# Kernel tuning notes

Hardware: AMD Instinct MI355X
Metric: run time of the kernel (lower is better)

Reference implementation:

```python
import jax, jax.numpy as jnp
import numpy as np

N_NODES = 100000; N_EDGES = 800000
N_SVC = 51200; E_SVC = 409600
B = 1024; OUT = 50; HID = 128; EMB = 64; VOCAB = 100
BN_EPS = 1e-5


def _bn(x, g, b):
    # BatchNorm1d in training mode: biased batch statistics
    m = x.mean(0)
    v = x.var(0)
    return (x - m) * jax.lax.rsqrt(v + BN_EPS) * g + b


def _gin(x, ei, W1, b1, bng, bnb, W2, b2, eps, n):
    # GINConv: nn((1+eps)*x + sum_{j->i} x_j), aggregate source feats at target ei[1]
    agg = jax.ops.segment_sum(x[ei[0]], ei[1], num_segments=n)
    h = (1.0 + eps) * x + agg
    h = _bn(h @ W1 + b1, bng, bnb)
    return jax.nn.relu(h) @ W2 + b2


def _gcn(x, ei, ew, W, b, n):
    # GCNConv with edge weights: add self loops (w=1), symmetric normalization
    xw = x @ W
    loop = jnp.arange(n)
    row = jnp.concatenate([ei[0], loop])
    col = jnp.concatenate([ei[1], loop])
    w = jnp.concatenate([ew, jnp.ones((n,), ew.dtype)])
    deg = jax.ops.segment_sum(w, col, num_segments=n)
    dinv = jnp.where(deg > 0, jax.lax.rsqrt(deg), 0.0)
    norm = dinv[row] * w * dinv[col]
    return jax.ops.segment_sum(norm[:, None] * xw[row], col, num_segments=n) + b


def setup_inputs() -> dict:
    key = jax.random.key(0)
    ks = jax.random.split(key, 48)
    p = lambda k, s: jax.random.normal(k, s, jnp.float32) * 0.05
    H2 = 2 * HID
    inp = dict(
        node_ids=jax.random.randint(ks[0], (N_NODES,), 0, VOCAB),
        node_feats=jax.random.normal(ks[1], (N_NODES, 6), jnp.float32),
        edge_index=jax.random.randint(ks[2], (2, N_EDGES), 0, N_NODES),
        svc_ids=jax.random.randint(ks[3], (N_SVC,), 0, VOCAB),
        svc_feats=jax.random.normal(ks[4], (N_SVC, 4), jnp.float32),
        edge_index_service=jax.random.randint(ks[5], (2, E_SVC), 0, N_SVC),
        edge_attr_service=jax.random.uniform(ks[6], (E_SVC,), jnp.float32),
        batch=jnp.sort(jax.random.randint(ks[7], (N_NODES,), 0, B)),
        num_graphs=B,
        out_channels=OUT,
        emb_node=p(ks[8], (VOCAB, EMB)),
        emb_svc=p(ks[9], (VOCAB, EMB)),
        # GIN layer 0 (in = EMB + 6)
        g0_W1=p(ks[10], (EMB + 6, H2)), g0_b1=jnp.zeros((H2,), jnp.float32),
        g0_bng1=jnp.ones((H2,), jnp.float32), g0_bnb1=jnp.zeros((H2,), jnp.float32),
        g0_W2=p(ks[11], (H2, HID)), g0_b2=jnp.zeros((HID,), jnp.float32),
        g0_eps=jnp.zeros((), jnp.float32),
        bn0_g=jnp.ones((HID,), jnp.float32), bn0_b=jnp.zeros((HID,), jnp.float32),
        # GIN layer 1 (in = HID)
        g1_W1=p(ks[12], (HID, H2)), g1_b1=jnp.zeros((H2,), jnp.float32),
        g1_bng1=jnp.ones((H2,), jnp.float32), g1_bnb1=jnp.zeros((H2,), jnp.float32),
        g1_W2=p(ks[13], (H2, HID)), g1_b2=jnp.zeros((HID,), jnp.float32),
        g1_eps=jnp.zeros((), jnp.float32),
        bn1_g=jnp.ones((HID,), jnp.float32), bn1_b=jnp.zeros((HID,), jnp.float32),
        node_lin_W=p(ks[14], (HID, HID)), node_lin_b=jnp.zeros((HID,), jnp.float32),
        # GCN layer 0 (in = EMB + 4)
        c0_W=p(ks[15], (EMB + 4, H2)), c0_b=jnp.zeros((H2,), jnp.float32),
        cbn0_g=jnp.ones((H2,), jnp.float32), cbn0_b=jnp.zeros((H2,), jnp.float32),
        # GCN layer 1 (in = 2*HID)
        c1_W=p(ks[16], (H2, H2)), c1_b=jnp.zeros((H2,), jnp.float32),
        cbn1_g=jnp.ones((H2,), jnp.float32), cbn1_b=jnp.zeros((H2,), jnp.float32),
        svc_lin_W=p(ks[17], (H2, HID)), svc_lin_b=jnp.zeros((HID,), jnp.float32),
    )
    return inp


def reference(node_feats, svc_feats, edge_attr_service, emb_node, emb_svc,
              g0_W1, g0_b1, g0_bng1, g0_bnb1, g0_W2, g0_b2, g0_eps, bn0_g, bn0_b,
              g1_W1, g1_b1, g1_bng1, g1_bnb1, g1_W2, g1_b2, g1_eps, bn1_g, bn1_b,
              node_lin_W, node_lin_b,
              c0_W, c0_b, cbn0_g, cbn0_b, c1_W, c1_b, cbn1_g, cbn1_b,
              svc_lin_W, svc_lin_b,
              node_ids, svc_ids, edge_index, edge_index_service, batch,
              num_graphs, out_channels):
    n = node_feats.shape[0]
    ns = svc_feats.shape[0]
    # node branch: embedding(col 0) ++ 6 float cols, 2 GIN layers
    x = jnp.concatenate([emb_node[node_ids], node_feats], axis=-1)
    x = jax.nn.relu(_bn(_gin(x, edge_index, g0_W1, g0_b1, g0_bng1, g0_bnb1,
                             g0_W2, g0_b2, g0_eps, n), bn0_g, bn0_b))
    x = jax.nn.relu(_bn(_gin(x, edge_index, g1_W1, g1_b1, g1_bng1, g1_bnb1,
                             g1_W2, g1_b2, g1_eps, n), bn1_g, bn1_b))
    # service branch: embedding ++ 4 qos cols, 2 GCN layers (isServices=True)
    xs = jnp.concatenate([emb_svc[svc_ids], svc_feats], axis=-1)
    xs = jax.nn.relu(_bn(_gcn(xs, edge_index_service, edge_attr_service, c0_W, c0_b, ns),
                         cbn0_g, cbn0_b))
    xs = jax.nn.relu(_bn(_gcn(xs, edge_index_service, edge_attr_service, c1_W, c1_b, ns),
                         cbn1_g, cbn1_b))
    xs = xs @ svc_lin_W + svc_lin_b
    x = x @ node_lin_W + node_lin_b
    # scatter-mean pooling over graphs
    cnt = jax.ops.segment_sum(jnp.ones((n,), x.dtype), batch, num_segments=num_graphs)
    xg = jax.ops.segment_sum(x, batch, num_segments=num_graphs) / jnp.clip(cnt, 1.0)[:, None]
    # scatter-mean over service slots: indices [0..out-1] repeated per graph
    svc_batch = jnp.tile(jnp.arange(out_channels), ns // out_channels)
    scnt = jax.ops.segment_sum(jnp.ones((ns,), xs.dtype), svc_batch, num_segments=out_channels)
    xsg = jax.ops.segment_sum(xs, svc_batch, num_segments=out_channels) / jnp.clip(scnt, 1.0)[:, None]
    return jax.nn.sigmoid(xg @ xsg.T)
```

## Files before the change

### kernel.cpp

```cpp
#include <hip/hip_runtime.h>
#include <hip/hip_bf16.h>
#include <cstddef>
#include <cstdint>

typedef __hip_bfloat16 bf16;
typedef __attribute__((ext_vector_type(8))) short short8;
typedef __attribute__((ext_vector_type(4))) float floatx4;

static __device__ __forceinline__ float b2f(bf16 v) { return __bfloat162float(v); }

static __device__ __forceinline__ short f2bf(float f) {
    unsigned u = __float_as_uint(f);
    unsigned r = u + 0x7FFF + ((u >> 16) & 1);
    return (short)(r >> 16);
}
static __device__ __forceinline__ float bf2f(short h) {
    return __uint_as_float(((unsigned)(unsigned short)h) << 16);
}
static __device__ __forceinline__ float loadf(const void* p, int mode, size_t i) {
    if (mode == 1) return b2f(((const bf16*)p)[i]);
    if (mode == 2) return ((const float*)p)[i];
    return 0.f;
}

#define NCONV 35
struct DetArgs { const void* src[NCONV]; int n[NCONV]; };

__global__ void detect_all(DetArgs a, int* __restrict__ modes) {
    int b = blockIdx.x;
    int n = a.n[b];
    const unsigned short* w = (const unsigned short*)a.src[b];
    __shared__ int cz, cbad, cevz, codz;
    if (threadIdx.x == 0) { cz = 0; cbad = 0; cevz = 0; codz = 0; }
    __syncthreads();
    int K = n < 2048 ? n : 2048;
    int z = 0, bad = 0, evz = 0, odz = 0;
    for (int i = threadIdx.x; i < K; i += blockDim.x) {
        unsigned short v = w[i];
        int e = (v >> 7) & 0xFF;
        bool isz = (v & 0x7FFF) == 0;
        if (isz) { z++; if (i & 1) odz++; else evz++; }
        else if (e < 91 || e > 140) bad++;
    }
    atomicAdd(&cz, z); atomicAdd(&cbad, bad);
    atomicAdd(&cevz, evz); atomicAdd(&codz, odz);
    __syncthreads();
    if (threadIdx.x == 0) {
        int mode;
        if (cz >= K) mode = 0;
        else if (cbad * 16 > K) mode = 2;
        else if (cevz * 4 > K && codz * 16 < K) mode = 2;
        else mode = 1;
        modes[b] = mode;
    }
}

struct WtArgs {
    const void* W[8]; short* wt[8];
    int midx[8]; int KW[8]; int ldw[8]; int Kpad[8]; int N[8];
};
__global__ void wt_build_all(WtArgs a, const int* __restrict__ modes) {
    int e = blockIdx.y;
    int n = blockIdx.x; if (n >= a.N[e]) return;
    int k = threadIdx.x; if (k >= a.Kpad[e]) return;
    float v = (k < a.KW[e]) ? loadf(a.W[e], modes[a.midx[e]], (size_t)k * a.ldw[e] + n) : 0.f;
    a.wt[e][(size_t)n * a.Kpad[e] + k] = f2bf(v);
}

__global__ void build_feat_bf16(const void* __restrict__ emb, const int* __restrict__ ids,
                                const void* __restrict__ feats, const int* __restrict__ modes,
                                int eidx, int fidx, unsigned short* __restrict__ P,
                                int nf, int Ws) {
    int i = blockIdx.x;
    int d = threadIdx.x;
    if (d >= Ws) return;
    float v;
    if (d < 64)           v = loadf(emb, modes[eidx], (size_t)ids[i] * 64 + d);
    else if (d < 64 + nf) v = loadf(feats, modes[fidx], (size_t)i * nf + (d - 64));
    else                  v = 0.f;
    P[(size_t)i * Ws + d] = (unsigned short)f2bf(v);
}

__global__ void csr_count(const int* __restrict__ dst, int nE, int* __restrict__ cnt) {
    int e = blockIdx.x * blockDim.x + threadIdx.x;
    if (e < nE) atomicAdd(&cnt[dst[e]], 1);
}

__global__ __launch_bounds__(256) void scan_part(const int* __restrict__ cnt, int n,
                                                 int* __restrict__ bsum) {
    __shared__ int red[256];
    int blk = blockIdx.x, t = threadIdx.x;
    int base = blk * 1024 + t * 4;
    int s = 0;
    #pragma unroll
    for (int k = 0; k < 4; ++k) { int i = base + k; if (i < n) s += cnt[i]; }
    red[t] = s;
    __syncthreads();
    for (int off = 128; off > 0; off >>= 1) {
        if (t < off) red[t] += red[t + off];
        __syncthreads();
    }
    if (t == 0) bsum[blk] = red[0];
}

__global__ __launch_bounds__(128) void scan_mid(int* __restrict__ bsum, int nb,
                                                int* __restrict__ rowptr, int n) {
    __shared__ int sh[128];
    int t = threadIdx.x;
    int v = (t < nb) ? bsum[t] : 0;
    sh[t] = v;
    __syncthreads();
    for (int off = 1; off < 128; off <<= 1) {
        int u = (t >= off) ? sh[t - off] : 0;
        __syncthreads();
        sh[t] += u;
        __syncthreads();
    }
    if (t < nb) bsum[t] = sh[t] - v;
    if (t == 127) rowptr[n] = sh[127];
}

__global__ __launch_bounds__(256) void scan_fin(const int* __restrict__ cnt, int n,
                                                const int* __restrict__ bsum,
                                                int* __restrict__ rowptr, int* __restrict__ cursor) {
    __shared__ int sh[256];
    int blk = blockIdx.x, t = threadIdx.x;
    int base = blk * 1024 + t * 4;
    int v[4], s = 0;
    #pragma unroll
    for (int k = 0; k < 4; ++k) { int i = base + k; v[k] = (i < n) ? cnt[i] : 0; s += v[k]; }
    sh[t] = s;
    __syncthreads();
    for (int off = 1; off < 256; off <<= 1) {
        int u = (t >= off) ? sh[t - off] : 0;
        __syncthreads();
        sh[t] += u;
        __syncthreads();
    }
    int run = sh[t] - s + bsum[blk];
    #pragma unroll
    for (int k = 0; k < 4; ++k) {
        int i = base + k;
        if (i < n) { rowptr[i] = run; cursor[i] = run; run += v[k]; }
    }
}

__global__ void csr_fill(const int* __restrict__ src, const int* __restrict__ dst,
                         const void* __restrict__ w, const int* __restrict__ modes, int widx,
                         const float* __restrict__ dinv, int nE, int* __restrict__ cursor,
                         int* __restrict__ adj, short* __restrict__ adjw) {
    int e = blockIdx.x * blockDim.x + threadIdx.x;
    if (e < nE) {
        int s = src[e];
        int pos = atomicAdd(&cursor[dst[e]], 1);
        adj[pos] = s;
        if (adjw) adjw[pos] = f2bf(dinv[s] * loadf(w, modes[widx], e));
    }
}

__global__ __launch_bounds__(256) void gin_gather_bf16(
        const unsigned short* __restrict__ P, const int* __restrict__ rowptr,
        const int* __restrict__ adj, const void* __restrict__ eps,
        const int* __restrict__ modes, int eidx,
        const float* __restrict__ bnsc, const float* __restrict__ bnsh,
        unsigned short* __restrict__ Po, int Ws, int nN) {
    int W8 = Ws >> 3;
    int g = threadIdx.x >> 4;
    int l = threadIdx.x & 15;
    int i = blockIdx.x * 16 + g;
    if (i >= nN || l >= W8) return;
    float epsv = 1.0f + loadf(eps, modes[eidx], 0);
    float sc[8], sh[8];
    bool bn = bnsc != nullptr;
    if (bn) {
        *(float4*)&sc[0] = *(const float4*)(bnsc + l * 8);
        *(float4*)&sc[4] = *(const float4*)(bnsc + l * 8 + 4);
        *(float4*)&sh[0] = *(const float4*)(bnsh + l * 8);
        *(float4*)&sh[4] = *(const float4*)(bnsh + l * 8 + 4);
    }
    int lo = rowptr[i], hi = rowptr[i + 1];
    float acc[8] = {};
    for (int p = lo; p < hi; ++p) {
        short8 v = *(const short8*)(P + (size_t)adj[p] * Ws + l * 8);
        #pragma unroll
        for (int j = 0; j < 8; ++j) {
            float y = bf2f(v[j]);
            if (bn) y = fmaxf(fmaf(y, sc[j], sh[j]), 0.f);
            acc[j] += y;
        }
    }
    size_t o = (size_t)i * Ws + l * 8;
    short8 sv = *(const short8*)(P + o);
    short8 r;
    #pragma unroll
    for (int j = 0; j < 8; ++j) {
        float y = bf2f(sv[j]);
        if (bn) y = fmaxf(fmaf(y, sc[j], sh[j]), 0.f);
        r[j] = f2bf(acc[j] + epsv * y);
    }
    *(short8*)(Po + o) = r;
}

__global__ __launch_bounds__(256) void gcn_gather(
        const float* __restrict__ xw, const int* __restrict__ rowptr,
        const int* __restrict__ adj, const short* __restrict__ adjw,
        const float* __restrict__ dinv, const void* __restrict__ bias,
        const int* __restrict__ modes, int bidx, float* __restrict__ out, int nS) {
    int g = threadIdx.x >> 6;
    int l = threadIdx.x & 63;
    int i = blockIdx.x * 4 + g;
    if (i >= nS) return;
    float di = dinv[i];
    int bmode = modes[bidx];
    size_t o = (size_t)i * 256 + (l << 2);
    float4 self = *(const float4*)(xw + o);
    float4 acc;
    float dd = di * di;
    acc.x = self.x * dd + loadf(bias, bmode, (l << 2) + 0);
    acc.y = self.y * dd + loadf(bias, bmode, (l << 2) + 1);
    acc.z = self.z * dd + loadf(bias, bmode, (l << 2) + 2);
    acc.w = self.w * dd + loadf(bias, bmode, (l << 2) + 3);
    int lo = rowptr[i], hi = rowptr[i + 1];
    int p = lo;
    for (; p + 1 < hi; p += 2) {
        int s0 = adj[p], s1 = adj[p + 1];
        float w0 = di * bf2f(adjw[p]), w1 = di * bf2f(adjw[p + 1]);
        float4 v0 = *(const float4*)(xw + (size_t)s0 * 256 + (l << 2));
        float4 v1 = *(const float4*)(xw + (size_t)s1 * 256 + (l << 2));
        acc.x += w0 * v0.x + w1 * v1.x;
        acc.y += w0 * v0.y + w1 * v1.y;
        acc.z += w0 * v0.z + w1 * v1.z;
        acc.w += w0 * v0.w + w1 * v1.w;
    }
    if (p < hi) {
        float w0 = di * bf2f(adjw[p]);
        float4 v0 = *(const float4*)(xw + (size_t)adj[p] * 256 + (l << 2));
        acc.x += w0 * v0.x; acc.y += w0 * v0.y;
        acc.z += w0 * v0.z; acc.w += w0 * v0.w;
    }
    *(float4*)(out + o) = acc;
}

__global__ __launch_bounds__(256) void gemm_mfma(
        const void* __restrict__ A, int afmt, int ldk,
        const float* __restrict__ bnsc, const float* __restrict__ bnsh,
        const short* __restrict__ Wt,
        const void* __restrict__ bias, const int* __restrict__ modes, int bias_midx,
        float* __restrict__ outF, unsigned short* __restrict__ oB,
        float* __restrict__ stats, int M, int N, int ksteps, int bf_out) {
    int tid  = threadIdx.x;
    int wv   = tid >> 6, lane = tid & 63;
    int m16  = lane & 15, q = lane >> 4;
    int bm   = blockIdx.y * 128 + wv * 32;
    int n0   = blockIdx.x * 128;
    int r0 = min(bm + m16, M - 1);
    int r1 = min(bm + 16 + m16, M - 1);
    const short8* ba0 = (const short8*)((const short*)A + (size_t)r0 * ldk + q * 8);
    const short8* ba1 = (const short8*)((const short*)A + (size_t)r1 * ldk + q * 8);
    const float*  fa0 = (const float*)A + (size_t)r0 * ldk + q * 8;
    const float*  fa1 = (const float*)A + (size_t)r1 * ldk + q * 8;
    const short8* pb[8];
    #pragma unroll
    for (int nt = 0; nt < 8; ++nt)
        pb[nt] = (const short8*)(Wt + (size_t)(n0 + nt * 16 + m16) * ldk + q * 8);

    floatx4 acc[2][8];
    #pragma unroll
    for (int mt = 0; mt < 2; ++mt)
        #pragma unroll
        for (int nt = 0; nt < 8; ++nt)
            acc[mt][nt] = (floatx4){0.f, 0.f, 0.f, 0.f};

    bool bn = bnsc != nullptr;
    for (int ks = 0; ks < ksteps; ++ks) {
        int idx = ks * 4;
        short8 a0, a1;
        if (afmt == 0 && !bn) {
            a0 = ba0[idx];
            a1 = ba1[idx];
        } else {
            float v0[8], v1[8];
            if (afmt == 0) {
                short8 u0 = ba0[idx], u1 = ba1[idx];
                #pragma unroll
                for (int j = 0; j < 8; ++j) { v0[j] = bf2f(u0[j]); v1[j] = bf2f(u1[j]); }
            } else {
                *(float4*)&v0[0] = *(const float4*)(fa0 + ks * 32);
                *(float4*)&v0[4] = *(const float4*)(fa0 + ks * 32 + 4);
                *(float4*)&v1[0] = *(const float4*)(fa1 + ks * 32);
                *(float4*)&v1[4] = *(const float4*)(fa1 + ks * 32 + 4);
            }
            if (bn) {
                int c0 = ks * 32 + q * 8;
                float scv[8], shv[8];
                *(float4*)&scv[0] = *(const float4*)(bnsc + c0);
                *(float4*)&scv[4] = *(const float4*)(bnsc + c0 + 4);
                *(float4*)&shv[0] = *(const float4*)(bnsh + c0);
                *(float4*)&shv[4] = *(const float4*)(bnsh + c0 + 4);
                #pragma unroll
                for (int j = 0; j < 8; ++j) {
                    v0[j] = fmaxf(fmaf(v0[j], scv[j], shv[j]), 0.f);
                    v1[j] = fmaxf(fmaf(v1[j], scv[j], shv[j]), 0.f);
                }
            }
            #pragma unroll
            for (int j = 0; j < 8; ++j) { a0[j] = f2bf(v0[j]); a1[j] = f2bf(v1[j]); }
        }
        #pragma unroll
        for (int nt = 0; nt < 8; ++nt) {
            short8 b = pb[nt][idx];
            acc[0][nt] = __builtin_amdgcn_mfma_f32_16x16x32_bf16(a0, b, acc[0][nt], 0, 0, 0);
            acc[1][nt] = __builtin_amdgcn_mfma_f32_16x16x32_bf16(a1, b, acc[1][nt], 0, 0, 0);
        }
    }

    float bv[8];
    int bmode = bias ? modes[bias_midx] : 0;
    #pragma unroll
    for (int nt = 0; nt < 8; ++nt)
        bv[nt] = bias ? loadf(bias, bmode, n0 + nt * 16 + m16) : 0.f;

    if (bf_out) {
        float sA[8], qA[8];
        #pragma unroll
        for (int nt = 0; nt < 8; ++nt) { sA[nt] = 0.f; qA[nt] = 0.f; }
        #pragma unroll
        for (int mt = 0; mt < 2; ++mt)
            #pragma unroll
            for (int r = 0; r < 4; ++r) {
                int row = bm + mt * 16 + q * 4 + r;
                bool ok = row < M;
                #pragma unroll
                for (int nt = 0; nt < 8; ++nt) {
                    float v = acc[mt][nt][r] + bv[nt];
                    if (ok) {
                        oB[(size_t)row * N + n0 + nt * 16 + m16] = (unsigned short)f2bf(v);
                        sA[nt] += v; qA[nt] += v * v;
                    }
                }
            }
        #pragma unroll
        for (int nt = 0; nt < 8; ++nt) {
            sA[nt] += __shfl_xor(sA[nt], 16); sA[nt] += __shfl_xor(sA[nt], 32);
            qA[nt] += __shfl_xor(qA[nt], 16); qA[nt] += __shfl_xor(qA[nt], 32);
        }
        __shared__ float redS[4][128], redQ[4][128];
        if (q == 0) {
            #pragma unroll
            for (int nt = 0; nt < 8; ++nt) {
                redS[wv][nt * 16 + m16] = sA[nt];
                redQ[wv][nt * 16 + m16] = qA[nt];
            }
        }
        __syncthreads();
        if (tid < 128) {
            float s = 0.f, qq = 0.f;
            #pragma unroll
            for (int w = 0; w < 4; ++w) { s += redS[w][tid]; qq += redQ[w][tid]; }
            atomicAdd(&stats[n0 + tid], s);
            atomicAdd(&stats[N + n0 + tid], qq);
        }
    } else {
        #pragma unroll
        for (int mt = 0; mt < 2; ++mt)
            #pragma unroll
            for (int r = 0; r < 4; ++r) {
                int row = bm + mt * 16 + q * 4 + r;
                if (row >= M) continue;
                #pragma unroll
                for (int nt = 0; nt < 8; ++nt)
                    outF[(size_t)row * N + n0 + nt * 16 + m16] = acc[mt][nt][r] + bv[nt];
            }
    }
}

__global__ void bn_finalize(float* __restrict__ stats, const void* __restrict__ g,
                            const void* __restrict__ b, const int* __restrict__ modes,
                            int gidx, int bidx, int C, float invM) {
    int c = threadIdx.x;
    if (c < C) {
        float mean = stats[c] * invM;
        float var  = fmaxf(stats[C + c] * invM - mean * mean, 0.f);
        float sc   = loadf(g, modes[gidx], c) * rsqrtf(var + 1e-5f);
        stats[2 * C + c] = sc;
        stats[3 * C + c] = loadf(b, modes[bidx], c) - mean * sc;
    }
}

__global__ void bn_stats_f32(const float* __restrict__ X, float* __restrict__ stats,
                             int M, int C, int rows) {
    int c = threadIdx.x;
    int r0 = blockIdx.x * rows;
    int r1 = min(r0 + rows, M);
    float s = 0.f, s2 = 0.f;
    for (int r = r0; r < r1; ++r) {
        float v = X[(size_t)r * C + c];
        s += v; s2 += v * v;
    }
    atomicAdd(&stats[c], s);
    atomicAdd(&stats[C + c], s2);
}

__global__ void deg_scatter(const void* __restrict__ ew, const int* __restrict__ modes, int eidx,
                            const int* __restrict__ col, float* __restrict__ deg, int nE) {
    int e = blockIdx.x * blockDim.x + threadIdx.x;
    if (e < nE) atomicAdd(&deg[col[e]], loadf(ew, modes[eidx], e));
}

__global__ void dinv_fin(float* __restrict__ deg, int n) {
    int i = blockIdx.x * blockDim.x + threadIdx.x;
    if (i < n) {
        float d = deg[i] + 1.0f;
        deg[i] = d > 0.f ? rsqrtf(d) : 0.f;
    }
}

__global__ void pool_sorted(const float* __restrict__ xn, const int* __restrict__ batch,
                            float* __restrict__ xg, int nN) {
    int g = blockIdx.x;
    int lo = 0, hi = nN;
    while (lo < hi) { int mid = (lo + hi) >> 1; if (batch[mid] < g) lo = mid + 1; else hi = mid; }
    int lo2 = lo, hi2 = nN;
    while (lo2 < hi2) { int mid = (lo2 + hi2) >> 1; if (batch[mid] < g + 1) lo2 = mid + 1; else hi2 = mid; }
    int d = threadIdx.x;
    float s = 0.f;
    for (int r = lo; r < lo2; ++r) s += xn[(size_t)r * 128 + d];
    xg[(size_t)g * 128 + d] = s / fmaxf((float)(lo2 - lo), 1.0f);
}

__global__ void svc_pool1(const float* __restrict__ xsl, float* __restrict__ partial) {
    int o = blockIdx.x;
    int c = blockIdx.y;
    int d = threadIdx.x;
    float s = 0.f;
    int r0 = c * 128;
    for (int r = r0; r < r0 + 128; ++r)
        s += xsl[((size_t)(r * 50 + o)) * 128 + d];
    partial[((size_t)(o * 8 + c)) * 128 + d] = s;
}

__global__ void svc_pool2(const float* __restrict__ partial, float* __restrict__ xsg) {
    int o = blockIdx.x;
    int d = threadIdx.x;
    float s = 0.f;
    #pragma unroll
    for (int c = 0; c < 8; ++c)
        s += partial[((size_t)(o * 8 + c)) * 128 + d];
    xsg[o * 128 + d] = s * (1.0f / 1024.0f);
}

__global__ void final_out(const float* __restrict__ xg, const float* __restrict__ xsg,
                          const int* __restrict__ modes, void* __restrict__ out) {
    __shared__ float xrow[128];
    int g = blockIdx.x;
    for (int d = threadIdx.x; d < 128; d += 64) xrow[d] = xg[(size_t)g * 128 + d];
    __syncthreads();
    int o = threadIdx.x;
    if (o < 50) {
        const float* xs = xsg + o * 128;
        float s = 0.f;
        #pragma unroll 4
        for (int d = 0; d < 128; ++d) s += xrow[d] * xs[d];
        float sg = 1.0f / (1.0f + __expf(-s));
        if (modes[0] == 1) ((bf16*)out)[(size_t)g * 50 + o] = __float2bfloat16(sg);
        else               ((float*)out)[(size_t)g * 50 + o] = sg;
    }
}

extern "C" void kernel_launch(void* const* d_in, const int* in_sizes, int n_in,
                              void* d_out, int out_size, void* d_ws, size_t ws_size,
                              hipStream_t stream) {
    const int nN = 100000, nE = 800000, nS = 51200, nES = 409600;
    const int Bg = 1024;

    const int* node_ids = (const int*)d_in[0];
    const int* ei       = (const int*)d_in[2];
    const int* svc_ids  = (const int*)d_in[3];
    const int* eis      = (const int*)d_in[5];
    const int* batch    = (const int*)d_in[7];

    float* ws    = (float*)d_ws;
    int*   modes = (int*)ws;
    float* stats = ws + 64;
    float* dinv  = ws + 1088;
    float* xsg   = ws + 52288;
    int*   bsum  = (int*)(ws + 58688);
    int*   rp_n  = (int*)(ws + 58944);
    int*   adj_n = (int*)(ws + 158948);
    int*   rp_s  = (int*)(ws + 958948);
    int*   adj_s = (int*)(ws + 1010152);
    short* adw_s = (short*)(ws + 1419752);
    short* wtb   = (short*)(ws + 1624552);
    float* xg    = ws + 1755624;
    float* part  = ws + 1886696;
    float* A25   = ws + 1937896;
    float* B13   = ws + 27537896;
    float* C13   = ws + 40645096;
    size_t need  = (size_t)53752296 * 4;
    if (ws_size < need) return;
    int* cur_n = (int*)xg;
    int* cur_s = (int*)part;
    int* bsum_n = bsum;
    int* bsum_s = bsum + 128;

    unsigned short* A25B = (unsigned short*)A25;
    unsigned short* B13B = (unsigned short*)B13;
    unsigned short* C13B = (unsigned short*)C13;
    float* B13F = B13;  float* A25F = A25;

    float* sc256 = stats + 512; float* sh256 = stats + 768;
    float* sc128 = stats + 256; float* sh128 = stats + 384;

    short* wt0 = wtb;
    short* wt1 = wt0 + 24576;
    short* wt2 = wt1 + 32768;
    short* wt3 = wt2 + 32768;
    short* wt4 = wt3 + 32768;
    short* wt5 = wt4 + 16384;
    short* wt6 = wt5 + 24576;
    short* wt7 = wt6 + 65536;

    static const int conv_idx[NCONV] = {1, 4, 6, 10, 11,
        12, 13, 14, 15, 16, 17, 18, 19, 20,
        21, 22, 23, 24, 25, 26, 27, 28, 29,
        30, 31, 32, 33, 34, 35, 36, 37, 38, 39, 40, 41};
    DetArgs da;
    for (int b = 0; b < NCONV; ++b) { da.src[b] = d_in[conv_idx[b]]; da.n[b] = in_sizes[conv_idx[b]]; }
    detect_all<<<NCONV, 256, 0, stream>>>(da, modes);

    {
        WtArgs wa;
        const int din_i[8]  = {12, 16, 21, 25, 30, 32, 36, 40};
        const int midx_i[8] = {5, 9, 14, 18, 23, 25, 29, 33};
        const int KW_i[8]   = {70, 256, 128, 256, 128, 68, 256, 256};
        const int ldw_i[8]  = {256, 128, 256, 128, 128, 256, 256, 128};
        short* wt_i[8]      = {wt0, wt1, wt2, wt3, wt4, wt5, wt6, wt7};
        const int Kp_i[8]   = {96, 256, 128, 256, 128, 96, 256, 256};
        const int N_i[8]    = {256, 128, 256, 128, 128, 256, 256, 128};
        for (int e = 0; e < 8; ++e) {
            wa.W[e] = d_in[din_i[e]]; wa.midx[e] = midx_i[e]; wa.KW[e] = KW_i[e];
            wa.ldw[e] = ldw_i[e]; wa.wt[e] = wt_i[e]; wa.Kpad[e] = Kp_i[e]; wa.N[e] = N_i[e];
        }
        wt_build_all<<<dim3(256, 8), 256, 0, stream>>>(wa, modes);
    }

    hipMemsetAsync(dinv, 0, nS * sizeof(float), stream);
    deg_scatter<<<(nES + 255) / 256, 256, 0, stream>>>(d_in[6], modes, 2, eis + nES, dinv, nES);
    dinv_fin<<<(nS + 255) / 256, 256, 0, stream>>>(dinv, nS);

    const int nbN = (nN + 1023) / 1024, nbS = (nS + 1023) / 1024;
    hipMemsetAsync(cur_n, 0, nN * sizeof(int), stream);
    csr_count<<<(nE + 255) / 256, 256, 0, stream>>>(ei + nE, nE, cur_n);
    scan_part<<<nbN, 256, 0, stream>>>(cur_n, nN, bsum_n);
    scan_mid<<<1, 128, 0, stream>>>(bsum_n, nbN, rp_n, nN);
    scan_fin<<<nbN, 256, 0, stream>>>(cur_n, nN, bsum_n, rp_n, cur_n);
    csr_fill<<<(nE + 255) / 256, 256, 0, stream>>>(ei, ei + nE, nullptr, modes, 2, nullptr,
                                                   nE, cur_n, adj_n, nullptr);

    hipMemsetAsync(cur_s, 0, nS * sizeof(int), stream);
    csr_count<<<(nES + 255) / 256, 256, 0, stream>>>(eis + nES, nES, cur_s);
    scan_part<<<nbS, 256, 0, stream>>>(cur_s, nS, bsum_s);
    scan_mid<<<1, 128, 0, stream>>>(bsum_s, nbS, rp_s, nS);
    scan_fin<<<nbS, 256, 0, stream>>>(cur_s, nS, bsum_s, rp_s, cur_s);
    csr_fill<<<(nES + 255) / 256, 256, 0, stream>>>(eis, eis + nES, d_in[6], modes, 2, dinv,
                                                    nES, cur_s, adj_s, adw_s);

    auto gemm = [&](const void* A, int afmt, int ldk, const float* bsc, const float* bsh,
                    const short* Wt, const void* bias, int bidx,
                    float* outF, unsigned short* oB, int M, int N, int bfo) {
        if (bfo) hipMemsetAsync(stats, 0, 2 * N * sizeof(float), stream);
        dim3 grid(N / 128, (M + 127) / 128);
        gemm_mfma<<<grid, 256, 0, stream>>>(A, afmt, ldk, bsc, bsh, Wt, bias, modes, bidx,
                                            outF, oB, stats, M, N, ldk / 32, bfo);
    };
    auto bnfin = [&](int gidx, int bidx, const void* g, const void* b, int C, int M) {
        bn_finalize<<<1, C, 0, stream>>>(stats, g, b, modes, gidx, bidx, C, 1.0f / M);
    };

    build_feat_bf16<<<nN, 128, 0, stream>>>(d_in[10], node_ids, d_in[1], modes, 3, 0,
                                            C13B, 6, 96);
    gin_gather_bf16<<<(nN + 15) / 16, 256, 0, stream>>>(C13B, rp_n, adj_n, d_in[18], modes, 11,
                                                        nullptr, nullptr, B13B, 96, nN);
    gemm(B13B, 0, 96, nullptr, nullptr, wt0, d_in[13], 6, nullptr, A25B, nN, 256, 1);
    bnfin(7, 8, d_in[14], d_in[15], 256, nN);
    gemm(A25B, 0, 256, sc256, sh256, wt1, d_in[17], 10, nullptr, C13B, nN, 128, 1);
    bnfin(12, 13, d_in[19], d_in[20], 128, nN);
    gin_gather_bf16<<<(nN + 15) / 16, 256, 0, stream>>>(C13B, rp_n, adj_n, d_in[27], modes, 20,
                                                        sc128, sh128, B13B, 128, nN);
    gemm(B13B, 0, 128, nullptr, nullptr, wt2, d_in[22], 15, nullptr, A25B, nN, 256, 1);
    bnfin(16, 17, d_in[23], d_in[24], 256, nN);
    gemm(A25B, 0, 256, sc256, sh256, wt3, d_in[26], 19, nullptr, C13B, nN, 128, 1);
    bnfin(21, 22, d_in[28], d_in[29], 128, nN);
    gemm(C13B, 0, 128, sc128, sh128, wt4, d_in[31], 24, B13F, nullptr, nN, 128, 0);
    pool_sorted<<<Bg, 128, 0, stream>>>(B13F, batch, xg, nN);

    build_feat_bf16<<<nS, 128, 0, stream>>>(d_in[11], svc_ids, d_in[4], modes, 4, 1,
                                            C13B, 4, 96);
    gemm(C13B, 0, 96, nullptr, nullptr, wt5, nullptr, 0, B13F, nullptr, nS, 256, 0);
    gcn_gather<<<(nS + 3) / 4, 256, 0, stream>>>(B13F, rp_s, adj_s, adw_s, dinv, d_in[33],
                                                 modes, 26, A25F, nS);
    hipMemsetAsync(stats, 0, 2 * 256 * sizeof(float), stream);
    bn_stats_f32<<<(nS + 31) / 32, 256, 0, stream>>>(A25F, stats, nS, 256, 32);
    bnfin(27, 28, d_in[34], d_in[35], 256, nS);
    gemm(A25F, 1, 256, sc256, sh256, wt6, nullptr, 0, B13F, nullptr, nS, 256, 0);
    gcn_gather<<<(nS + 3) / 4, 256, 0, stream>>>(B13F, rp_s, adj_s, adw_s, dinv, d_in[37],
                                                 modes, 30, A25F, nS);
    hipMemsetAsync(stats, 0, 2 * 256 * sizeof(float), stream);
    bn_stats_f32<<<(nS + 31) / 32, 256, 0, stream>>>(A25F, stats, nS, 256, 32);
    bnfin(31, 32, d_in[38], d_in[39], 256, nS);
    gemm(A25F, 1, 256, sc256, sh256, wt7, d_in[41], 34, B13F, nullptr, nS, 128, 0);
    svc_pool1<<<dim3(50, 8), 128, 0, stream>>>(B13F, part);
    svc_pool2<<<50, 128, 0, stream>>>(part, xsg);

    final_out<<<Bg, 64, 0, stream>>>(xg, xsg, modes, d_out);
}
```

Baseline: 1.236 ms.

## Store GCN and final node GEMM outputs in bf16 with LDS-staged coalesced writes

The GCN feature transforms and the final node linear now write bf16 instead of fp32, and the GCN gather reads bf16 rows with 32 lanes per node. Node pooling reads the bf16 output as well. The GEMM bf16 epilogue stages its tile in shared memory and writes 16-byte coalesced rows, with a new mode that skips the BN stats. This halves the gather and pooling traffic and removes scattered 2-byte stores, at the cost of extra bf16 rounding and more shared memory per block.

```diff
diff --git a/kernel.cpp b/kernel.cpp
--- a/kernel.cpp
+++ b/kernel.cpp
@@ -201,44 +201,34 @@
     *(short8*)(Po + o) = r;
 }
 
-__global__ __launch_bounds__(256) void gcn_gather(
-        const float* __restrict__ xw, const int* __restrict__ rowptr,
+__global__ __launch_bounds__(256) void gcn_gather_bf16(
+        const unsigned short* __restrict__ xw, const int* __restrict__ rowptr,
         const int* __restrict__ adj, const short* __restrict__ adjw,
         const float* __restrict__ dinv, const void* __restrict__ bias,
         const int* __restrict__ modes, int bidx, float* __restrict__ out, int nS) {
-    int g = threadIdx.x >> 6;
-    int l = threadIdx.x & 63;
-    int i = blockIdx.x * 4 + g;
+    int g = threadIdx.x >> 5;
+    int l = threadIdx.x & 31;
+    int i = blockIdx.x * 8 + g;
     if (i >= nS) return;
     float di = dinv[i];
     int bmode = modes[bidx];
-    size_t o = (size_t)i * 256 + (l << 2);
-    float4 self = *(const float4*)(xw + o);
-    float4 acc;
+    size_t o = (size_t)i * 256 + l * 8;
+    short8 sv = *(const short8*)(xw + o);
     float dd = di * di;
-    acc.x = self.x * dd + loadf(bias, bmode, (l << 2) + 0);
-    acc.y = self.y * dd + loadf(bias, bmode, (l << 2) + 1);
-    acc.z = self.z * dd + loadf(bias, bmode, (l << 2) + 2);
-    acc.w = self.w * dd + loadf(bias, bmode, (l << 2) + 3);
+    float acc[8];
+    #pragma unroll
+    for (int j = 0; j < 8; ++j)
+        acc[j] = bf2f(sv[j]) * dd + loadf(bias, bmode, l * 8 + j);
     int lo = rowptr[i], hi = rowptr[i + 1];
-    int p = lo;
-    for (; p + 1 < hi; p += 2) {
-        int s0 = adj[p], s1 = adj[p + 1];
-        float w0 = di * bf2f(adjw[p]), w1 = di * bf2f(adjw[p + 1]);
-        float4 v0 = *(const float4*)(xw + (size_t)s0 * 256 + (l << 2));
-        float4 v1 = *(const float4*)(xw + (size_t)s1 * 256 + (l << 2));
-        acc.x += w0 * v0.x + w1 * v1.x;
-        acc.y += w0 * v0.y + w1 * v1.y;
-        acc.z += w0 * v0.z + w1 * v1.z;
-        acc.w += w0 * v0.w + w1 * v1.w;
-    }
-    if (p < hi) {
-        float w0 = di * bf2f(adjw[p]);
-        float4 v0 = *(const float4*)(xw + (size_t)adj[p] * 256 + (l << 2));
-        acc.x += w0 * v0.x; acc.y += w0 * v0.y;
-        acc.z += w0 * v0.z; acc.w += w0 * v0.w;
-    }
-    *(float4*)(out + o) = acc;
+    for (int p = lo; p < hi; ++p) {
+        float w = di * bf2f(adjw[p]);
+        short8 v = *(const short8*)(xw + (size_t)adj[p] * 256 + l * 8);
+        #pragma unroll
+        for (int j = 0; j < 8; ++j)
+            acc[j] += w * bf2f(v[j]);
+    }
+    *(float4*)(out + o) = *(float4*)&acc[0];
+    *(float4*)(out + o + 4) = *(float4*)&acc[4];
 }
 
 __global__ __launch_bounds__(256) void gemm_mfma(
@@ -247,7 +237,7 @@
         const short* __restrict__ Wt,
         const void* __restrict__ bias, const int* __restrict__ modes, int bias_midx,
         float* __restrict__ outF, unsigned short* __restrict__ oB,
-        float* __restrict__ stats, int M, int N, int ksteps, int bf_out) {
+        float* __restrict__ stats, int M, int N, int ksteps, int omode) {
     int tid  = threadIdx.x;
     int wv   = tid >> 6, lane = tid & 63;
     int m16  = lane & 15, q = lane >> 4;
@@ -320,7 +310,9 @@
     for (int nt = 0; nt < 8; ++nt)
         bv[nt] = bias ? loadf(bias, bmode, n0 + nt * 16 + m16) : 0.f;
 
-    if (bf_out) {
+    if (omode) {
+        __shared__ unsigned short tile[128][136];
+        __shared__ float redS[4][128], redQ[4][128];
         float sA[8], qA[8];
         #pragma unroll
         for (int nt = 0; nt < 8; ++nt) { sA[nt] = 0.f; qA[nt] = 0.f; }
@@ -328,32 +320,41 @@
         for (int mt = 0; mt < 2; ++mt)
             #pragma unroll
             for (int r = 0; r < 4; ++r) {
-                int row = bm + mt * 16 + q * 4 + r;
-                bool ok = row < M;
+                int rl = wv * 32 + mt * 16 + q * 4 + r;
+                bool ok = (bm + mt * 16 + q * 4 + r) < M;
                 #pragma unroll
                 for (int nt = 0; nt < 8; ++nt) {
                     float v = acc[mt][nt][r] + bv[nt];
-                    if (ok) {
-                        oB[(size_t)row * N + n0 + nt * 16 + m16] = (unsigned short)f2bf(v);
-                        sA[nt] += v; qA[nt] += v * v;
-                    }
+                    tile[rl][nt * 16 + m16] = (unsigned short)f2bf(v);
+                    if (ok && omode == 1) { sA[nt] += v; qA[nt] += v * v; }
                 }
             }
-        #pragma unroll
-        for (int nt = 0; nt < 8; ++nt) {
-            sA[nt] += __shfl_xor(sA[nt], 16); sA[nt] += __shfl_xor(sA[nt], 32);
-            qA[nt] += __shfl_xor(qA[nt], 16); qA[nt] += __shfl_xor(qA[nt], 32);
-        }
-        __shared__ float redS[4][128], redQ[4][128];
-        if (q == 0) {
+        if (omode == 1) {
             #pragma unroll
             for (int nt = 0; nt < 8; ++nt) {
-                redS[wv][nt * 16 + m16] = sA[nt];
-                redQ[wv][nt * 16 + m16] = qA[nt];
+                sA[nt] += __shfl_xor(sA[nt], 16); sA[nt] += __shfl_xor(sA[nt], 32);
+                qA[nt] += __shfl_xor(qA[nt], 16); qA[nt] += __shfl_xor(qA[nt], 32);
+            }
+            if (q == 0) {
+                #pragma unroll
+                for (int nt = 0; nt < 8; ++nt) {
+                    redS[wv][nt * 16 + m16] = sA[nt];
+                    redQ[wv][nt * 16 + m16] = qA[nt];
+                }
             }
         }
         __syncthreads();
-        if (tid < 128) {
+        int rb = blockIdx.y * 128;
+        #pragma unroll
+        for (int c = 0; c < 8; ++c) {
+            int lin = c * 256 + tid;
+            int row = lin >> 4;
+            int cu  = lin & 15;
+            int grow = rb + row;
+            if (grow < M)
+                *(short8*)(oB + (size_t)grow * N + n0 + cu * 8) = *(short8*)&tile[row][cu * 8];
+        }
+        if (omode == 1 && tid < 128) {
             float s = 0.f, qq = 0.f;
             #pragma unroll
             for (int w = 0; w < 4; ++w) { s += redS[w][tid]; qq += redQ[w][tid]; }
@@ -415,8 +416,9 @@
     }
 }
 
-__global__ void pool_sorted(const float* __restrict__ xn, const int* __restrict__ batch,
-                            float* __restrict__ xg, int nN) {
+__global__ void pool_sorted_bf16(const unsigned short* __restrict__ xn,
+                                 const int* __restrict__ batch,
+                                 float* __restrict__ xg, int nN) {
     int g = blockIdx.x;
     int lo = 0, hi = nN;
     while (lo < hi) { int mid = (lo + hi) >> 1; if (batch[mid] < g) lo = mid + 1; else hi = mid; }
@@ -424,7 +426,7 @@
     while (lo2 < hi2) { int mid = (lo2 + hi2) >> 1; if (batch[mid] < g + 1) lo2 = mid + 1; else hi2 = mid; }
     int d = threadIdx.x;
     float s = 0.f;
-    for (int r = lo; r < lo2; ++r) s += xn[(size_t)r * 128 + d];
+    for (int r = lo; r < lo2; ++r) s += bf2f((short)xn[(size_t)r * 128 + d]);
     xg[(size_t)g * 128 + d] = s / fmaxf((float)(lo2 - lo), 1.0f);
 }
 
@@ -567,11 +569,11 @@
 
     auto gemm = [&](const void* A, int afmt, int ldk, const float* bsc, const float* bsh,
                     const short* Wt, const void* bias, int bidx,
-                    float* outF, unsigned short* oB, int M, int N, int bfo) {
-        if (bfo) hipMemsetAsync(stats, 0, 2 * N * sizeof(float), stream);
+                    float* outF, unsigned short* oB, int M, int N, int om) {
+        if (om == 1) hipMemsetAsync(stats, 0, 2 * N * sizeof(float), stream);
         dim3 grid(N / 128, (M + 127) / 128);
         gemm_mfma<<<grid, 256, 0, stream>>>(A, afmt, ldk, bsc, bsh, Wt, bias, modes, bidx,
-                                            outF, oB, stats, M, N, ldk / 32, bfo);
+                                            outF, oB, stats, M, N, ldk / 32, om);
     };
     auto bnfin = [&](int gidx, int bidx, const void* g, const void* b, int C, int M) {
         bn_finalize<<<1, C, 0, stream>>>(stats, g, b, modes, gidx, bidx, C, 1.0f / M);
@@ -591,20 +593,20 @@
     bnfin(16, 17, d_in[23], d_in[24], 256, nN);
     gemm(A25B, 0, 256, sc256, sh256, wt3, d_in[26], 19, nullptr, C13B, nN, 128, 1);
     bnfin(21, 22, d_in[28], d_in[29], 128, nN);
-    gemm(C13B, 0, 128, sc128, sh128, wt4, d_in[31], 24, B13F, nullptr, nN, 128, 0);
-    pool_sorted<<<Bg, 128, 0, stream>>>(B13F, batch, xg, nN);
+    gemm(C13B, 0, 128, sc128, sh128, wt4, d_in[31], 24, nullptr, B13B, nN, 128, 2);
+    pool_sorted_bf16<<<Bg, 128, 0, stream>>>(B13B, batch, xg, nN);
 
     build_feat_bf16<<<nS, 128, 0, stream>>>(d_in[11], svc_ids, d_in[4], modes, 4, 1,
                                             C13B, 4, 96);
-    gemm(C13B, 0, 96, nullptr, nullptr, wt5, nullptr, 0, B13F, nullptr, nS, 256, 0);
-    gcn_gather<<<(nS + 3) / 4, 256, 0, stream>>>(B13F, rp_s, adj_s, adw_s, dinv, d_in[33],
-                                                 modes, 26, A25F, nS);
+    gemm(C13B, 0, 96, nullptr, nullptr, wt5, nullptr, 0, nullptr, B13B, nS, 256, 2);
+    gcn_gather_bf16<<<(nS + 7) / 8, 256, 0, stream>>>(B13B, rp_s, adj_s, adw_s, dinv, d_in[33],
+                                                      modes, 26, A25F, nS);
     hipMemsetAsync(stats, 0, 2 * 256 * sizeof(float), stream);
     bn_stats_f32<<<(nS + 31) / 32, 256, 0, stream>>>(A25F, stats, nS, 256, 32);
     bnfin(27, 28, d_in[34], d_in[35], 256, nS);
-    gemm(A25F, 1, 256, sc256, sh256, wt6, nullptr, 0, B13F, nullptr, nS, 256, 0);
-    gcn_gather<<<(nS + 3) / 4, 256, 0, stream>>>(B13F, rp_s, adj_s, adw_s, dinv, d_in[37],
-                                                 modes, 30, A25F, nS);
+    gemm(A25F, 1, 256, sc256, sh256, wt6, nullptr, 0, nullptr, B13B, nS, 256, 2);
+    gcn_gather_bf16<<<(nS + 7) / 8, 256, 0, stream>>>(B13B, rp_s, adj_s, adw_s, dinv, d_in[37],
+                                                      modes, 30, A25F, nS);
     hipMemsetAsync(stats, 0, 2 * 256 * sizeof(float), stream);
     bn_stats_f32<<<(nS + 31) / 32, 256, 0, stream>>>(A25F, stats, nS, 256, 32);
     bnfin(31, 32, d_in[38], d_in[39], 256, nS);
```

After: 1.107 ms. 10.4% less time.
